# Optimization experiments

Hardware: AMD Instinct MI355X
Metric: run time of the kernel (lower is better)

Reference implementation:

```python
import jax, jax.numpy as jnp
import numpy as np

STRIDE, PAD, DIL, DG = 1, 1, 1, 1
KH, KW = 3, 3


def setup_inputs() -> dict:
    key = jax.random.key(0)
    k1, k2, k3 = jax.random.split(key, 3)
    B, Cin, H, W, Cout = 8, 128, 64, 64, 256
    Ho = (H + 2 * PAD - (DIL * (KH - 1) + 1)) // STRIDE + 1
    Wo = (W + 2 * PAD - (DIL * (KW - 1) + 1)) // STRIDE + 1
    x = jax.random.normal(k1, (B, Cin, H, W), jnp.float32)
    offset = jax.random.normal(k2, (B, DG * 2 * KH * KW, Ho, Wo), jnp.float32)
    stdv = 1.0 / np.sqrt(Cin * KH * KW)
    weight = jax.random.uniform(k3, (Cout, Cin, KH, KW), jnp.float32, -stdv, stdv)
    return {"x": x, "offset": offset, "weight": weight}


def deform_conv2d(x, offset, weight, stride=STRIDE, pad=PAD, dil=DIL, dg=DG):
    """Deformable conv v1: per-tap learned offsets + bilinear gather + GEMM."""
    B, C, H, W = x.shape
    Co, Ci, kh, kw = weight.shape
    K = kh * kw
    cg = C // dg  # channels per deformable group
    Ho = (H + 2 * pad - (dil * (kh - 1) + 1)) // stride + 1
    Wo = (W + 2 * pad - (dil * (kw - 1) + 1)) // stride + 1

    # offset layout: [B, dg*K*2, Ho, Wo] with (dy, dx) interleaved per tap
    off = offset.reshape(B, dg, K, 2, Ho, Wo)

    # base sampling positions per output pixel and kernel tap
    ky, kx = jnp.meshgrid(jnp.arange(kh), jnp.arange(kw), indexing="ij")
    base_y = (jnp.arange(Ho) * stride - pad)[None, :, None] + (ky.reshape(K) * dil)[:, None, None]  # [K,Ho,1]
    base_x = (jnp.arange(Wo) * stride - pad)[None, None, :] + (kx.reshape(K) * dil)[:, None, None]  # [K,1,Wo]

    py = base_y[None, None].astype(offset.dtype) + off[:, :, :, 0]  # [B,dg,K,Ho,Wo]
    px = base_x[None, None].astype(offset.dtype) + off[:, :, :, 1]  # [B,dg,K,Ho,Wo]

    y0f = jnp.floor(py)
    x0f = jnp.floor(px)
    fy = py - y0f
    fx = px - x0f
    y0 = y0f.astype(jnp.int32)
    x0 = x0f.astype(jnp.int32)
    y1 = y0 + 1
    x1 = x0 + 1

    x_flat = x.reshape(B, dg, cg, H * W)

    def corner(yi, xi, w):
        # zero out contributions whose corner falls outside the image
        valid = (yi >= 0) & (yi < H) & (xi >= 0) & (xi < W)
        idx = jnp.clip(yi, 0, H - 1) * W + jnp.clip(xi, 0, W - 1)  # [B,dg,K,Ho,Wo]
        g = jax.vmap(jax.vmap(lambda xf, i: xf[:, i]))(x_flat, idx)  # [B,dg,cg,K,Ho,Wo]
        return g * (w * valid)[:, :, None]

    cols = (corner(y0, x0, (1 - fy) * (1 - fx))
            + corner(y0, x1, (1 - fy) * fx)
            + corner(y1, x0, fy * (1 - fx))
            + corner(y1, x1, fy * fx))  # [B,dg,cg,K,Ho,Wo]

    w_r = weight.reshape(Co, dg, cg, K)
    return jnp.einsum("bgckhw,ogck->bohw", cols, w_r)


def reference(x, offset, weight):
    return deform_conv2d(x, offset, weight)
```

## Files before the change

kernel.cpp:

```cpp
#include <hip/hip_runtime.h>
#include <hip/hip_bf16.h>

#define CIN   128
#define HH    64
#define WW    64
#define COUT  256
#define HO    64
#define WO    64
#define NTAP  9
#define KTOT  (CIN*NTAP)
#define BK    32
#define NSTEP (KTOT/BK)
#define NB    8
#define CROW  272

typedef __attribute__((ext_vector_type(8))) short bf16x8;
typedef __attribute__((ext_vector_type(4))) short bf16x4;
typedef __attribute__((ext_vector_type(4))) float f32x4;

struct __align__(16) TapEntry {
  int   i00, i01, i10, i11;
  float w00, w01, w10, w11;
};

static __device__ __forceinline__ ushort f2bf(float v) {
  unsigned u = __float_as_uint(v);
  unsigned rnd = 0x7fffu + ((u >> 16) & 1u);
  return (ushort)((u + rnd) >> 16);
}
static __device__ __forceinline__ float bf2f(short s) {
  return __uint_as_float(((unsigned)(unsigned short)s) << 16);
}

__global__ __launch_bounds__(256) void prep(const float* __restrict__ x,
                                            const float* __restrict__ w,
                                            ushort* __restrict__ xt,
                                            ushort* __restrict__ wbt) {
  const int blk = blockIdx.x;
  const int tid = threadIdx.x;
  if (blk < NB * HH) {
    const int b = blk >> 6, y = blk & 63;
    const int px = tid & 63, c8 = tid >> 6;
    const float* src = x + (size_t)b * CIN * HH * WW + y * WW + px;
    ushort* dst = xt + (((size_t)(b * HH + y) * WW) + px) * CIN;
    #pragma unroll
    for (int cc = 0; cc < 4; ++cc) {
      const int c0 = cc * 32 + c8 * 8;
      bf16x8 v;
      #pragma unroll
      for (int j = 0; j < 8; ++j)
        v[j] = (short)f2bf(src[(size_t)(c0 + j) * (HH * WW)]);
      *reinterpret_cast<bf16x8*>(dst + c0) = v;
    }
  } else {
    const int h = (blk - NB * HH) * 256 + tid;
    const int s   = h >> 10;
    const int c16 = (h >> 6) & 15;
    const int l   = h & 63;
    const int q   = l >> 4;
    const int r   = l & 15;
    const int co  = c16 * 16 + r;
    const int tap = s >> 2;
    const int ci0 = (s & 3) * 32 + q * 8;
    bf16x8 o;
    #pragma unroll
    for (int j = 0; j < 8; ++j)
      o[j] = (short)f2bf(w[(size_t)(co * CIN + ci0 + j) * NTAP + tap]);
    *reinterpret_cast<bf16x8*>(wbt + (size_t)h * 8) = o;
  }
}

__global__ __launch_bounds__(256, 2)
void dcn5(const ushort* __restrict__ xt, const float* __restrict__ off,
          const ushort* __restrict__ wbt, float* __restrict__ out)
{
  __shared__ TapEntry taps[NTAP * WO];
  __shared__ __align__(16) char colsB[WO * CROW];

  const int tid = threadIdx.x;
  const int b  = blockIdx.x & 7;
  const int ho = blockIdx.x >> 3;

  for (int e = tid; e < NTAP * WO; e += 256) {
    const int k  = e >> 6;
    const int wo = e & 63;
    const float* op = off + (((size_t)(b * 18 + 2 * k) * HO + ho) * WO + wo);
    const float dy = op[0];
    const float dx = op[HO * WO];
    const float py  = (float)(ho - 1 + (k / 3)) + dy;
    const float pxf = (float)(wo - 1 + (k % 3)) + dx;
    const float y0f = floorf(py), x0f = floorf(pxf);
    const float fy = py - y0f, fx = pxf - x0f;
    const int y0 = (int)y0f, x0 = (int)x0f;
    const int y1 = y0 + 1,  x1 = x0 + 1;
    const bool vy0 = (unsigned)y0 < HH, vy1 = (unsigned)y1 < HH;
    const bool vx0 = (unsigned)x0 < WW, vx1 = (unsigned)x1 < WW;
    const int cy0 = min(max(y0, 0), HH - 1), cy1 = min(max(y1, 0), HH - 1);
    const int cx0 = min(max(x0, 0), WW - 1), cx1 = min(max(x1, 0), WW - 1);
    TapEntry t;
    t.i00 = (cy0 * WW + cx0) << 8;  t.i01 = (cy0 * WW + cx1) << 8;
    t.i10 = (cy1 * WW + cx0) << 8;  t.i11 = (cy1 * WW + cx1) << 8;
    const float gy = 1.f - fy, gx = 1.f - fx;
    t.w00 = (vy0 && vx0) ? gy * gx : 0.f;
    t.w01 = (vy0 && vx1) ? gy * fx : 0.f;
    t.w10 = (vy1 && vx0) ? fy * gx : 0.f;
    t.w11 = (vy1 && vx1) ? fy * fx : 0.f;
    taps[e] = t;
  }

  const int lane = tid & 63;
  const int grp  = tid >> 6;
  const int l15  = lane & 15;
  const int q    = lane >> 4;
  const int g    = q;
  const int s16  = l15;

  f32x4 acc[4][4];
  #pragma unroll
  for (int m = 0; m < 4; ++m)
    #pragma unroll
    for (int n = 0; n < 4; ++n)
      acc[m][n] = 0.f;

  const char* xb = reinterpret_cast<const char*>(xt)
                 + (size_t)b * (HH * WW * CIN * 2) + s16 * 16;

  __syncthreads();

  #pragma unroll 1
  for (int tap = 0; tap < NTAP; ++tap) {
    bf16x8 hv[4];
    #pragma unroll
    for (int pq = 0; pq < 4; ++pq) {
      const int px = (grp << 4) + (pq << 2) + g;
      const TapEntry te = taps[tap * WO + px];
      const bf16x8 c00 = *reinterpret_cast<const bf16x8*>(xb + te.i00);
      const bf16x8 c01 = *reinterpret_cast<const bf16x8*>(xb + te.i01);
      const bf16x8 c10 = *reinterpret_cast<const bf16x8*>(xb + te.i10);
      const bf16x8 c11 = *reinterpret_cast<const bf16x8*>(xb + te.i11);
      bf16x8 h;
      #pragma unroll
      for (int j = 0; j < 8; ++j) {
        const float v = te.w00 * bf2f(c00[j]) + te.w01 * bf2f(c01[j])
                      + te.w10 * bf2f(c10[j]) + te.w11 * bf2f(c11[j]);
        h[j] = (short)f2bf(v);
      }
      hv[pq] = h;
    }

    __syncthreads();

    #pragma unroll
    for (int pq = 0; pq < 4; ++pq) {
      const int px = (grp << 4) + (pq << 2) + g;
      *reinterpret_cast<bf16x8*>(colsB + px * CROW + s16 * 16) = hv[pq];
    }

    __syncthreads();

    #pragma unroll
    for (int kk = 0; kk < 4; ++kk) {
      const int s = tap * 4 + kk;
      bf16x8 a[4], bb[4];
      #pragma unroll
      for (int m = 0; m < 4; ++m)
        a[m] = *reinterpret_cast<const bf16x8*>(
            wbt + ((size_t)((s * 16 + grp * 4 + m) * 64 + lane)) * 8);
      #pragma unroll
      for (int n = 0; n < 4; ++n)
        bb[n] = *reinterpret_cast<const bf16x8*>(
            colsB + (n * 16 + l15) * CROW + kk * 64 + q * 16);
      #pragma unroll
      for (int m = 0; m < 4; ++m)
        #pragma unroll
        for (int n = 0; n < 4; ++n)
          acc[m][n] = __builtin_amdgcn_mfma_f32_16x16x32_bf16(
              a[m], bb[n], acc[m][n], 0, 0, 0);
    }
  }

  #pragma unroll
  for (int m = 0; m < 4; ++m)
    #pragma unroll
    for (int n = 0; n < 4; ++n)
      #pragma unroll
      for (int r = 0; r < 4; ++r) {
        const int co = grp * 64 + m * 16 + q * 4 + r;
        const int wo = n * 16 + l15;
        out[(((size_t)b * COUT + co) * HO + ho) * WO + wo] = acc[m][n][r];
      }
}

__global__ __launch_bounds__(256, 2)
void dcn_f32(const float* __restrict__ x, const float* __restrict__ off,
             const float* __restrict__ wgt, float* __restrict__ out)
{
  __shared__ TapEntry taps[NTAP * WO];
  __shared__ __align__(16) ushort colsf[WO * 40];
  const int tid = threadIdx.x;
  const int b  = blockIdx.x & 7;
  const int ho = blockIdx.x >> 3;
  for (int e = tid; e < NTAP * WO; e += 256) {
    const int k  = e >> 6;
    const int wo = e & 63;
    const float* op = off + (((size_t)(b * 18 + 2 * k) * HO + ho) * WO + wo);
    const float dy = op[0];
    const float dx = op[HO * WO];
    const float py  = (float)(ho - 1 + (k / 3)) + dy;
    const float pxf = (float)(wo - 1 + (k % 3)) + dx;
    const float y0f = floorf(py), x0f = floorf(pxf);
    const float fy = py - y0f, fx = pxf - x0f;
    const int y0 = (int)y0f, x0 = (int)x0f;
    const int y1 = y0 + 1,  x1 = x0 + 1;
    const bool vy0 = (unsigned)y0 < HH, vy1 = (unsigned)y1 < HH;
    const bool vx0 = (unsigned)x0 < WW, vx1 = (unsigned)x1 < WW;
    const int cy0 = min(max(y0, 0), HH - 1), cy1 = min(max(y1, 0), HH - 1);
    const int cx0 = min(max(x0, 0), WW - 1), cx1 = min(max(x1, 0), WW - 1);
    TapEntry t;
    t.i00 = cy0 * WW + cx0; t.i01 = cy0 * WW + cx1;
    t.i10 = cy1 * WW + cx0; t.i11 = cy1 * WW + cx1;
    const float gy = 1.f - fy, gx = 1.f - fx;
    t.w00 = (vy0 && vx0) ? gy * gx : 0.f;
    t.w01 = (vy0 && vx1) ? gy * fx : 0.f;
    t.w10 = (vy1 && vx0) ? fy * gx : 0.f;
    t.w11 = (vy1 && vx1) ? fy * fx : 0.f;
    taps[e] = t;
  }
  const int px = tid & 63, grp = tid >> 6, lane = tid & 63;
  const int l15 = lane & 15, q = lane >> 4;
  f32x4 acc[4][4];
  #pragma unroll
  for (int m = 0; m < 4; ++m)
    #pragma unroll
    for (int n = 0; n < 4; ++n) acc[m][n] = 0.f;
  const float* xb = x + (size_t)b * CIN * HH * WW;
  __syncthreads();
  for (int tap = 0; tap < NTAP; ++tap) {
    const TapEntry e = taps[tap * WO + px];
    for (int cb = 0; cb < 4; ++cb) {
      __syncthreads();
      {
        const float* xp = xb + (size_t)(cb * 32 + grp * 8) * (HH * WW);
        bf16x8 hv;
        #pragma unroll
        for (int j = 0; j < 8; ++j) {
          const float* p = xp + j * (HH * WW);
          const float v = e.w00 * p[e.i00] + e.w01 * p[e.i01]
                        + e.w10 * p[e.i10] + e.w11 * p[e.i11];
          hv[j] = (short)f2bf(v);
        }
        *reinterpret_cast<bf16x8*>(
            reinterpret_cast<char*>(colsf) + px * 80 + grp * 16) = hv;
      }
      __syncthreads();
      bf16x8 a[4], bbf[4];
      #pragma unroll
      for (int m = 0; m < 4; ++m) {
        const int co = grp * 64 + m * 16 + l15;
        bf16x8 t;
        #pragma unroll
        for (int j = 0; j < 8; ++j)
          t[j] = (short)f2bf(wgt[(size_t)(co * CIN + cb * 32 + q * 8 + j) * NTAP + tap]);
        a[m] = t;
      }
      #pragma unroll
      for (int n = 0; n < 4; ++n)
        bbf[n] = *reinterpret_cast<const bf16x8*>(
            reinterpret_cast<const char*>(colsf) + (n * 16 + l15) * 80 + q * 16);
      #pragma unroll
      for (int m = 0; m < 4; ++m)
        #pragma unroll
        for (int n = 0; n < 4; ++n)
          acc[m][n] = __builtin_amdgcn_mfma_f32_16x16x32_bf16(
              a[m], bbf[n], acc[m][n], 0, 0, 0);
    }
  }
  const int wco = grp * 64;
  #pragma unroll
  for (int m = 0; m < 4; ++m)
    #pragma unroll
    for (int n = 0; n < 4; ++n)
      #pragma unroll
      for (int r = 0; r < 4; ++r) {
        const int co = wco + m * 16 + q * 4 + r;
        const int wo = n * 16 + l15;
        out[(((size_t)b * COUT + co) * HO + ho) * WO + wo] = acc[m][n][r];
      }
}

extern "C" void kernel_launch(void* const* d_in, const int* in_sizes, int n_in,
                              void* d_out, int out_size, void* d_ws, size_t ws_size,
                              hipStream_t stream) {
  const float* x   = (const float*)d_in[0];
  const float* off = (const float*)d_in[1];
  const float* wgt = (const float*)d_in[2];
  float* out = (float*)d_out;

  const size_t xt_bytes = (size_t)NB * HH * WW * CIN * sizeof(ushort);
  const size_t wb_bytes = (size_t)NSTEP * COUT * BK * sizeof(ushort);
  if (ws_size >= xt_bytes + wb_bytes) {
    ushort* xtp  = (ushort*)d_ws;
    ushort* wbtp = (ushort*)((char*)d_ws + xt_bytes);
    const int wchunks = NSTEP * COUT * BK / 8;
    const int wblocks = wchunks / 256;
    prep<<<NB * HH + wblocks, 256, 0, stream>>>(x, wgt, xtp, wbtp);
    dcn5<<<NB * HO, 256, 0, stream>>>(xtp, off, wbtp, out);
  } else {
    dcn_f32<<<NB * HO, 256, 0, stream>>>(x, off, wgt, out);
  }
}
```

Baseline: 49.71 us.

## Double-buffer bilinear column tile to overlap gathers with MFMA

Adds a second shared-memory column buffer so the bilinear gather loads for the next tap are issued before the MFMA work of the current tap, with the combine and store into the other buffer done after the MFMAs. This cuts one of the two block barriers per tap and hides global gather latency behind matrix math. Weight fragments are also loaded two k-steps ahead in register double buffers. The cost is about 17KB more LDS and higher register pressure from holding 16 gathered vectors in flight, which could lower occupancy below the requested two blocks per CU.

```diff
diff --git a/kernel.cpp b/kernel.cpp
--- a/kernel.cpp
+++ b/kernel.cpp
@@ -13,6 +13,7 @@
 #define NSTEP (KTOT/BK)
 #define NB    8
 #define CROW  272
+#define CBUF  (WO*CROW)
 
 typedef __attribute__((ext_vector_type(8))) short bf16x8;
 typedef __attribute__((ext_vector_type(4))) short bf16x4;
@@ -30,6 +31,19 @@
 }
 static __device__ __forceinline__ float bf2f(short s) {
   return __uint_as_float(((unsigned)(unsigned short)s) << 16);
+}
+
+static __device__ __forceinline__ bf16x8 combine4(const bf16x8 c00, const bf16x8 c01,
+                                                  const bf16x8 c10, const bf16x8 c11,
+                                                  const f32x4 w) {
+  bf16x8 r;
+  #pragma unroll
+  for (int j = 0; j < 8; ++j) {
+    const float v = w.x * bf2f(c00[j]) + w.y * bf2f(c01[j])
+                  + w.z * bf2f(c10[j]) + w.w * bf2f(c11[j]);
+    r[j] = (short)f2bf(v);
+  }
+  return r;
 }
 
 __global__ __launch_bounds__(256) void prep(const float* __restrict__ x,
@@ -71,11 +85,11 @@
 }
 
 __global__ __launch_bounds__(256, 2)
-void dcn5(const ushort* __restrict__ xt, const float* __restrict__ off,
+void dcn6(const ushort* __restrict__ xt, const float* __restrict__ off,
           const ushort* __restrict__ wbt, float* __restrict__ out)
 {
   __shared__ TapEntry taps[NTAP * WO];
-  __shared__ __align__(16) char colsB[WO * CROW];
+  __shared__ __align__(16) char colsB[2 * CBUF];
 
   const int tid = threadIdx.x;
   const int b  = blockIdx.x & 7;
@@ -113,7 +127,7 @@
   const int l15  = lane & 15;
   const int q    = lane >> 4;
   const int g    = q;
-  const int s16  = l15;
+  const int s16b = l15 * 16;
 
   f32x4 acc[4][4];
   #pragma unroll
@@ -123,60 +137,95 @@
       acc[m][n] = 0.f;
 
   const char* xb = reinterpret_cast<const char*>(xt)
-                 + (size_t)b * (HH * WW * CIN * 2) + s16 * 16;
-
+                 + (size_t)b * (HH * WW * CIN * 2) + s16b;
+
+  __syncthreads();
+
+  bf16x8 c00[4], c01[4], c10[4], c11[4];
+  f32x4  tw[4];
+
+  #pragma unroll
+  for (int pq = 0; pq < 4; ++pq) {
+    const int px = (grp << 4) + (pq << 2) + g;
+    const TapEntry te = taps[px];
+    c00[pq] = *reinterpret_cast<const bf16x8*>(xb + te.i00);
+    c01[pq] = *reinterpret_cast<const bf16x8*>(xb + te.i01);
+    c10[pq] = *reinterpret_cast<const bf16x8*>(xb + te.i10);
+    c11[pq] = *reinterpret_cast<const bf16x8*>(xb + te.i11);
+    tw[pq]  = f32x4{te.w00, te.w01, te.w10, te.w11};
+  }
+  #pragma unroll
+  for (int pq = 0; pq < 4; ++pq) {
+    const int px = (grp << 4) + (pq << 2) + g;
+    const bf16x8 hv = combine4(c00[pq], c01[pq], c10[pq], c11[pq], tw[pq]);
+    *reinterpret_cast<bf16x8*>(colsB + px * CROW + s16b) = hv;
+  }
   __syncthreads();
 
   #pragma unroll 1
   for (int tap = 0; tap < NTAP; ++tap) {
-    bf16x8 hv[4];
-    #pragma unroll
-    for (int pq = 0; pq < 4; ++pq) {
-      const int px = (grp << 4) + (pq << 2) + g;
-      const TapEntry te = taps[tap * WO + px];
-      const bf16x8 c00 = *reinterpret_cast<const bf16x8*>(xb + te.i00);
-      const bf16x8 c01 = *reinterpret_cast<const bf16x8*>(xb + te.i01);
-      const bf16x8 c10 = *reinterpret_cast<const bf16x8*>(xb + te.i10);
-      const bf16x8 c11 = *reinterpret_cast<const bf16x8*>(xb + te.i11);
-      bf16x8 h;
-      #pragma unroll
-      for (int j = 0; j < 8; ++j) {
-        const float v = te.w00 * bf2f(c00[j]) + te.w01 * bf2f(c01[j])
-                      + te.w10 * bf2f(c10[j]) + te.w11 * bf2f(c11[j]);
-        h[j] = (short)f2bf(v);
-      }
-      hv[pq] = h;
+    const int cur = tap & 1;
+    const char* rbuf = colsB + cur * CBUF;
+    char*       wbuf = colsB + (cur ^ 1) * CBUF;
+    const bool  more = (tap + 1) < NTAP;
+
+    const ushort* aBase = wbt + ((size_t)((tap * 4 * 16 + grp * 4) * 64 + lane)) * 8;
+    #define ALOAD(kk, m) (*reinterpret_cast<const bf16x8*>(aBase + ((kk) * 16 + (m)) * 64 * 8))
+
+    bf16x8 a0[4], a1[4];
+    #pragma unroll
+    for (int m = 0; m < 4; ++m) { a0[m] = ALOAD(0, m); a1[m] = ALOAD(1, m); }
+
+    if (more) {
+      #pragma unroll
+      for (int pq = 0; pq < 4; ++pq) {
+        const int px = (grp << 4) + (pq << 2) + g;
+        const TapEntry te = taps[(tap + 1) * WO + px];
+        c00[pq] = *reinterpret_cast<const bf16x8*>(xb + te.i00);
+        c01[pq] = *reinterpret_cast<const bf16x8*>(xb + te.i01);
+        c10[pq] = *reinterpret_cast<const bf16x8*>(xb + te.i10);
+        c11[pq] = *reinterpret_cast<const bf16x8*>(xb + te.i11);
+        tw[pq]  = f32x4{te.w00, te.w01, te.w10, te.w11};
+      }
     }
 
+    bf16x8 bb[4];
+    #define BLOAD(kk) do { \
+      _Pragma("unroll") \
+      for (int n = 0; n < 4; ++n) \
+        bb[n] = *reinterpret_cast<const bf16x8*>( \
+            rbuf + (n * 16 + l15) * CROW + (kk) * 64 + q * 16); \
+    } while (0)
+    #define MFMA16(A) do { \
+      _Pragma("unroll") \
+      for (int m = 0; m < 4; ++m) \
+        _Pragma("unroll") \
+        for (int n = 0; n < 4; ++n) \
+          acc[m][n] = __builtin_amdgcn_mfma_f32_16x16x32_bf16( \
+              (A)[m], bb[n], acc[m][n], 0, 0, 0); \
+    } while (0)
+
+    BLOAD(0); MFMA16(a0);
+    #pragma unroll
+    for (int m = 0; m < 4; ++m) a0[m] = ALOAD(2, m);
+    BLOAD(1); MFMA16(a1);
+    #pragma unroll
+    for (int m = 0; m < 4; ++m) a1[m] = ALOAD(3, m);
+    BLOAD(2); MFMA16(a0);
+    BLOAD(3); MFMA16(a1);
+
+    if (more) {
+      #pragma unroll
+      for (int pq = 0; pq < 4; ++pq) {
+        const int px = (grp << 4) + (pq << 2) + g;
+        const bf16x8 hv = combine4(c00[pq], c01[pq], c10[pq], c11[pq], tw[pq]);
+        *reinterpret_cast<bf16x8*>(wbuf + px * CROW + s16b) = hv;
+      }
+    }
     __syncthreads();
-
-    #pragma unroll
-    for (int pq = 0; pq < 4; ++pq) {
-      const int px = (grp << 4) + (pq << 2) + g;
-      *reinterpret_cast<bf16x8*>(colsB + px * CROW + s16 * 16) = hv[pq];
-    }
-
-    __syncthreads();
-
-    #pragma unroll
-    for (int kk = 0; kk < 4; ++kk) {
-      const int s = tap * 4 + kk;
-      bf16x8 a[4], bb[4];
-      #pragma unroll
-      for (int m = 0; m < 4; ++m)
-        a[m] = *reinterpret_cast<const bf16x8*>(
-            wbt + ((size_t)((s * 16 + grp * 4 + m) * 64 + lane)) * 8);
-      #pragma unroll
-      for (int n = 0; n < 4; ++n)
-        bb[n] = *reinterpret_cast<const bf16x8*>(
-            colsB + (n * 16 + l15) * CROW + kk * 64 + q * 16);
-      #pragma unroll
-      for (int m = 0; m < 4; ++m)
-        #pragma unroll
-        for (int n = 0; n < 4; ++n)
-          acc[m][n] = __builtin_amdgcn_mfma_f32_16x16x32_bf16(
-              a[m], bb[n], acc[m][n], 0, 0, 0);
-    }
+    #undef ALOAD
+    #undef BLOAD
+    #undef MFMA16
   }
 
   #pragma unroll
@@ -304,7 +353,7 @@
     const int wchunks = NSTEP * COUT * BK / 8;
     const int wblocks = wchunks / 256;
     prep<<<NB * HH + wblocks, 256, 0, stream>>>(x, wgt, xtp, wbtp);
-    dcn5<<<NB * HO, 256, 0, stream>>>(xtp, off, wbtp, out);
+    dcn6<<<NB * HO, 256, 0, stream>>>(xtp, off, wbtp, out);
   } else {
     dcn_f32<<<NB * HO, 256, 0, stream>>>(x, off, wgt, out);
   }
```

Measured after the change: 50.57 us. About the same (+1.7%).

## Split tap reduction across two wave groups with LDS accumulator reduction

Applied to the files above, without the earlier changes.

The block grows from 256 to 512 threads. Two groups of four waves each handle a disjoint subset of kernel taps (5 and 4) using separate column buffers in LDS. The two partial accumulators are then summed through LDS before group 0 writes the output. This adds in-block parallelism along the K dimension so gather latency is hidden better. In exchange it uses more LDS per block, leaves group 1 idle in the last round because the 9 taps split unevenly, and adds reduction barriers.

```diff
diff --git a/kernel.cpp b/kernel.cpp
--- a/kernel.cpp
+++ b/kernel.cpp
@@ -13,6 +13,7 @@
 #define NSTEP (KTOT/BK)
 #define NB    8
 #define CROW  272
+#define CBUF  (WO*CROW)
 
 typedef __attribute__((ext_vector_type(8))) short bf16x8;
 typedef __attribute__((ext_vector_type(4))) short bf16x4;
@@ -70,18 +71,18 @@
   }
 }
 
-__global__ __launch_bounds__(256, 2)
-void dcn5(const ushort* __restrict__ xt, const float* __restrict__ off,
+__global__ __launch_bounds__(512, 4)
+void dcn7(const ushort* __restrict__ xt, const float* __restrict__ off,
           const ushort* __restrict__ wbt, float* __restrict__ out)
 {
   __shared__ TapEntry taps[NTAP * WO];
-  __shared__ __align__(16) char colsB[WO * CROW];
+  __shared__ __align__(16) char colsB[2 * CBUF];
 
   const int tid = threadIdx.x;
   const int b  = blockIdx.x & 7;
   const int ho = blockIdx.x >> 3;
 
-  for (int e = tid; e < NTAP * WO; e += 256) {
+  for (int e = tid; e < NTAP * WO; e += 512) {
     const int k  = e >> 6;
     const int wo = e & 63;
     const float* op = off + (((size_t)(b * 18 + 2 * k) * HO + ho) * WO + wo);
@@ -108,12 +109,14 @@
     taps[e] = t;
   }
 
-  const int lane = tid & 63;
-  const int grp  = tid >> 6;
-  const int l15  = lane & 15;
-  const int q    = lane >> 4;
-  const int g    = q;
-  const int s16  = l15;
+  const int w     = tid >> 6;
+  const int group = w >> 2;
+  const int grp   = w & 3;
+  const int lane  = tid & 63;
+  const int l15   = lane & 15;
+  const int q     = lane >> 4;
+  const int g     = q;
+  const int s16b  = l15 * 16;
 
   f32x4 acc[4][4];
   #pragma unroll
@@ -123,72 +126,99 @@
       acc[m][n] = 0.f;
 
   const char* xb = reinterpret_cast<const char*>(xt)
-                 + (size_t)b * (HH * WW * CIN * 2) + s16 * 16;
+                 + (size_t)b * (HH * WW * CIN * 2) + s16b;
+  char* mycols = colsB + group * CBUF;
 
   __syncthreads();
 
   #pragma unroll 1
-  for (int tap = 0; tap < NTAP; ++tap) {
-    bf16x8 hv[4];
-    #pragma unroll
-    for (int pq = 0; pq < 4; ++pq) {
-      const int px = (grp << 4) + (pq << 2) + g;
-      const TapEntry te = taps[tap * WO + px];
-      const bf16x8 c00 = *reinterpret_cast<const bf16x8*>(xb + te.i00);
-      const bf16x8 c01 = *reinterpret_cast<const bf16x8*>(xb + te.i01);
-      const bf16x8 c10 = *reinterpret_cast<const bf16x8*>(xb + te.i10);
-      const bf16x8 c11 = *reinterpret_cast<const bf16x8*>(xb + te.i11);
-      bf16x8 h;
-      #pragma unroll
-      for (int j = 0; j < 8; ++j) {
-        const float v = te.w00 * bf2f(c00[j]) + te.w01 * bf2f(c01[j])
-                      + te.w10 * bf2f(c10[j]) + te.w11 * bf2f(c11[j]);
-        h[j] = (short)f2bf(v);
-      }
-      hv[pq] = h;
-    }
+  for (int r = 0; r < 5; ++r) {
+    const int  tap    = group ? (5 + r) : r;
+    const bool active = group ? (r < 4) : true;
 
     __syncthreads();
 
-    #pragma unroll
-    for (int pq = 0; pq < 4; ++pq) {
-      const int px = (grp << 4) + (pq << 2) + g;
-      *reinterpret_cast<bf16x8*>(colsB + px * CROW + s16 * 16) = hv[pq];
+    if (active) {
+      #pragma unroll
+      for (int pq = 0; pq < 4; ++pq) {
+        const int px = (grp << 4) + (pq << 2) + g;
+        const TapEntry te = taps[tap * WO + px];
+        const bf16x8 c00 = *reinterpret_cast<const bf16x8*>(xb + te.i00);
+        const bf16x8 c01 = *reinterpret_cast<const bf16x8*>(xb + te.i01);
+        const bf16x8 c10 = *reinterpret_cast<const bf16x8*>(xb + te.i10);
+        const bf16x8 c11 = *reinterpret_cast<const bf16x8*>(xb + te.i11);
+        bf16x8 hv;
+        #pragma unroll
+        for (int j = 0; j < 8; ++j) {
+          const float v = te.w00 * bf2f(c00[j]) + te.w01 * bf2f(c01[j])
+                        + te.w10 * bf2f(c10[j]) + te.w11 * bf2f(c11[j]);
+          hv[j] = (short)f2bf(v);
+        }
+        *reinterpret_cast<bf16x8*>(mycols + px * CROW + s16b) = hv;
+      }
     }
 
     __syncthreads();
 
-    #pragma unroll
-    for (int kk = 0; kk < 4; ++kk) {
-      const int s = tap * 4 + kk;
-      bf16x8 a[4], bb[4];
-      #pragma unroll
-      for (int m = 0; m < 4; ++m)
-        a[m] = *reinterpret_cast<const bf16x8*>(
-            wbt + ((size_t)((s * 16 + grp * 4 + m) * 64 + lane)) * 8);
+    if (active) {
+      #pragma unroll
+      for (int kk = 0; kk < 4; ++kk) {
+        const int s = tap * 4 + kk;
+        bf16x8 a[4], bb[4];
+        #pragma unroll
+        for (int m = 0; m < 4; ++m)
+          a[m] = *reinterpret_cast<const bf16x8*>(
+              wbt + ((size_t)((s * 16 + grp * 4 + m) * 64 + lane)) * 8);
+        #pragma unroll
+        for (int n = 0; n < 4; ++n)
+          bb[n] = *reinterpret_cast<const bf16x8*>(
+              mycols + (n * 16 + l15) * CROW + kk * 64 + q * 16);
+        #pragma unroll
+        for (int m = 0; m < 4; ++m)
+          #pragma unroll
+          for (int n = 0; n < 4; ++n)
+            acc[m][n] = __builtin_amdgcn_mfma_f32_16x16x32_bf16(
+                a[m], bb[n], acc[m][n], 0, 0, 0);
+      }
+    }
+  }
+
+  f32x4* red = reinterpret_cast<f32x4*>(colsB);
+  const int t256 = tid & 255;
+  #pragma unroll
+  for (int p = 0; p < 2; ++p) {
+    __syncthreads();
+    if (group == 1) {
+      #pragma unroll
+      for (int m2 = 0; m2 < 2; ++m2)
+        #pragma unroll
+        for (int n = 0; n < 4; ++n)
+          red[(m2 * 4 + n) * 256 + t256] = acc[p * 2 + m2][n];
+    }
+    __syncthreads();
+    if (group == 0) {
+      #pragma unroll
+      for (int m2 = 0; m2 < 2; ++m2)
+        #pragma unroll
+        for (int n = 0; n < 4; ++n) {
+          const f32x4 v = red[(m2 * 4 + n) * 256 + t256];
+          acc[p * 2 + m2][n] += v;
+        }
+    }
+  }
+
+  if (group == 0) {
+    #pragma unroll
+    for (int m = 0; m < 4; ++m)
       #pragma unroll
       for (int n = 0; n < 4; ++n)
-        bb[n] = *reinterpret_cast<const bf16x8*>(
-            colsB + (n * 16 + l15) * CROW + kk * 64 + q * 16);
-      #pragma unroll
-      for (int m = 0; m < 4; ++m)
-        #pragma unroll
-        for (int n = 0; n < 4; ++n)
-          acc[m][n] = __builtin_amdgcn_mfma_f32_16x16x32_bf16(
-              a[m], bb[n], acc[m][n], 0, 0, 0);
-    }
-  }
-
-  #pragma unroll
-  for (int m = 0; m < 4; ++m)
-    #pragma unroll
-    for (int n = 0; n < 4; ++n)
-      #pragma unroll
-      for (int r = 0; r < 4; ++r) {
-        const int co = grp * 64 + m * 16 + q * 4 + r;
-        const int wo = n * 16 + l15;
-        out[(((size_t)b * COUT + co) * HO + ho) * WO + wo] = acc[m][n][r];
-      }
+        #pragma unroll
+        for (int rr = 0; rr < 4; ++rr) {
+          const int co = grp * 64 + m * 16 + q * 4 + rr;
+          const int wo = n * 16 + l15;
+          out[(((size_t)b * COUT + co) * HO + ho) * WO + wo] = acc[m][n][rr];
+        }
+  }
 }
 
 __global__ __launch_bounds__(256, 2)
@@ -304,7 +334,7 @@
     const int wchunks = NSTEP * COUT * BK / 8;
     const int wblocks = wchunks / 256;
     prep<<<NB * HH + wblocks, 256, 0, stream>>>(x, wgt, xtp, wbtp);
-    dcn5<<<NB * HO, 256, 0, stream>>>(xtp, off, wbtp, out);
+    dcn7<<<NB * HO, 512, 0, stream>>>(xtp, off, wbtp, out);
   } else {
     dcn_f32<<<NB * HO, 256, 0, stream>>>(x, off, wgt, out);
   }
```

Measured after the change: 56.16 us. 13.0% more time.
